# Performance work log

Hardware: AMD Instinct MI355X
Metric: run time of the kernel (lower is better)

## Reference

```python
import jax, jax.numpy as jnp
import numpy as np

N, D_MODEL, D_PE, H = 4096, 512, 16, 8


def setup_inputs() -> dict:
    key = jax.random.key(0)
    ks = jax.random.split(key, 6)
    s = 1.0 / np.sqrt(D_MODEL)
    return {
        "x": jax.random.normal(ks[0], (N, D_MODEL), dtype=jnp.float32),
        "pe": jax.random.normal(ks[1], (N, D_PE), dtype=jnp.float32),
        "w_qkv": jax.random.normal(ks[2], (D_MODEL, 3 * D_MODEL), dtype=jnp.float32) * s,
        "b_qkv": jnp.zeros((3 * D_MODEL,), dtype=jnp.float32),
        "w_pe": jax.random.normal(ks[3], (D_PE, H), dtype=jnp.float32) * (1.0 / np.sqrt(D_PE)),
        "b_pe": jnp.zeros((H,), dtype=jnp.float32),
        "w_out": jax.random.normal(ks[4], (D_MODEL, D_MODEL), dtype=jnp.float32) * s,
        "b_out": jnp.zeros((D_MODEL,), dtype=jnp.float32),
    }


def reference(x, pe, w_qkv, b_qkv, w_pe, b_pe, w_out, b_out):
    n, d = x.shape
    h = w_pe.shape[1]
    hd = d // h
    scale = hd ** -0.5

    qkv = (x @ w_qkv + b_qkv).reshape(n, 3, h, hd)  # [N,3,H,hd]
    q = jnp.transpose(qkv[:, 0], (1, 0, 2))  # [H,N,hd]
    k = jnp.transpose(qkv[:, 1], (1, 0, 2))
    v = jnp.transpose(qkv[:, 2], (1, 0, 2))

    pe_proj = pe @ w_pe + b_pe  # [N,H]
    # bias[h,i,j] = pe_proj[j,h] - pe_proj[i,h]  (matches torch unsqueeze/permute)
    pt = pe_proj.T  # [H,N]
    bias = pt[:, None, :] - pt[:, :, None]  # [H,N,N]

    scores = jnp.einsum('hnd,hmd->hnm', q, k) * scale + bias  # [H,N,N]
    attn = jax.nn.softmax(scores, axis=-1)
    out = jnp.einsum('hnm,hmd->hnd', attn, v)  # [H,N,hd]
    out = jnp.transpose(out, (1, 0, 2)).reshape(n, d)
    return out @ w_out + b_out
```

## Files before the change

### kernel.cpp

```cpp
#include <hip/hip_runtime.h>
#include <stdint.h>
#include <stddef.h>


typedef unsigned short u16;
typedef __attribute__((ext_vector_type(8))) short short8;
typedef __attribute__((ext_vector_type(8))) unsigned short us8;
typedef __attribute__((ext_vector_type(4))) unsigned short us4;
typedef __attribute__((ext_vector_type(4))) float floatx4;

__device__ __forceinline__ u16 f2b(float f) {
  union { float f; uint32_t u; } v; v.f = f;
  uint32_t u = v.u;
  return (u16)((u + 0x7fffu + ((u >> 16) & 1u)) >> 16);
}

__device__ __forceinline__ uint32_t pkbf16(float a, float b) {
  union { float f; uint32_t u; } x, y; x.f = a; y.f = b;
  return __builtin_amdgcn_perm(y.u + 0x8000u, x.u + 0x8000u, 0x07060302u);
}

#if __has_builtin(__builtin_amdgcn_exp2f)
__device__ __forceinline__ float fexp2(float x) { return __builtin_amdgcn_exp2f(x); }
#else
__device__ __forceinline__ float fexp2(float x) { return exp2f(x); }
#endif

__device__ __forceinline__ void gld16(const u16* g, u16* l) {
  __builtin_amdgcn_global_load_lds(
      (const __attribute__((address_space(1))) uint32_t*)(const void*)g,
      (__attribute__((address_space(3))) uint32_t*)(void*)l, 16, 0, 0);
}


__device__ __forceinline__ void tr_tile(const float* __restrict__ in,
                                        u16* __restrict__ out, int R, int C,
                                        int bx, int by, u16 (*tile)[33]) {
  int tx = threadIdx.x & 31, ty = threadIdx.x >> 5;
  int c0 = bx * 32, r0 = by * 32;
#pragma unroll
  for (int i = 0; i < 32; i += 8)
    tile[ty + i][tx] = f2b(in[(size_t)(r0 + ty + i) * C + c0 + tx]);
  __syncthreads();
#pragma unroll
  for (int i = 0; i < 32; i += 8)
    out[(size_t)(c0 + ty + i) * R + r0 + tx] = tile[tx][ty + i];
}

__global__ __launch_bounds__(256) void k_prep(
    const float* __restrict__ x, u16* __restrict__ xb,
    const float* __restrict__ w_qkv, u16* __restrict__ wqkvT,
    const float* __restrict__ w_out, u16* __restrict__ woutT,
    const float* __restrict__ pe, const float* __restrict__ w_pe,
    const float* __restrict__ b_pe, float* __restrict__ wexp,
    u16* __restrict__ wpb) {
  __shared__ u16 tile[32][33];
  int b = blockIdx.x;
  if (b < 2048) {
    int i = b * 256 + threadIdx.x;
    float4 v = ((const float4*)x)[i];
    uint2 o = make_uint2(pkbf16(v.x, v.y), pkbf16(v.z, v.w));
    ((uint2*)xb)[i] = o;
  } else if (b < 2816) {
    int idx = b - 2048;
    tr_tile(w_qkv, wqkvT, 512, 1536, idx % 48, idx / 48, tile);
  } else if (b < 3072) {
    int idx = b - 2816;
    tr_tile(w_out, woutT, 512, 512, idx % 16, idx / 16, tile);
  } else {
    int idx = (b - 3072) * 256 + threadIdx.x;
    int h = idx >> 12, n = idx & 4095;
    float acc = b_pe[h];
#pragma unroll
    for (int d = 0; d < 16; ++d) acc = fmaf(pe[n * 16 + d], w_pe[d * 8 + h], acc);
    float w = exp2f(acc * 1.4426950408889634f - 16.0f);
    u16 wb = f2b(w);
    union { uint32_t u; float f; } cv; cv.u = ((uint32_t)wb) << 16;
    wexp[h * 4096 + n] = cv.f;
    int pn = (n & ~31) | (((n >> 2) & 3) << 3) | (((n >> 4) & 1) << 2) | (n & 3);
    wpb[h * 4096 + pn] = wb;
  }
}


__global__ __launch_bounds__(512, 6) void k_gemm_qkv(const u16* __restrict__ A,
                                                     const u16* __restrict__ Bt,
                                                     const float* __restrict__ bias,
                                                     const float* __restrict__ wexp,
                                                     u16* __restrict__ qk,
                                                     u16* __restrict__ vtp) {
  __shared__ __align__(16) u16 smem[24576];
  const int tid = threadIdx.x;
  const int lane = tid & 63, wave = tid >> 6;
  const int colx = lane & 15, quad = lane >> 4;
  const int m0 = blockIdx.y * 64, n0 = blockIdx.x * 128;
  const int wm = wave >> 2, wn = wave & 3;
  const int sc = (lane & 7) ^ ((lane >> 3) & 7);
  const floatx4 fz = {0.f, 0.f, 0.f, 0.f};
  floatx4 acc[2][2];
#pragma unroll
  for (int i = 0; i < 2; ++i)
#pragma unroll
    for (int j = 0; j < 2; ++j) acc[i][j] = fz;

#define PREF_QKV(k0, b)                                                       \
  {                                                                           \
    int rowa = wave * 8 + (lane >> 3);                                        \
    gld16(&A[(size_t)(m0 + rowa) * 512 + (k0) + sc * 8],                      \
          &smem[(b) * 4096 + wave * 512 + lane * 8]);                         \
    _Pragma("unroll") for (int c = 0; c < 2; ++c) {                           \
      int rowb = wave * 16 + c * 8 + (lane >> 3);                             \
      gld16(&Bt[(size_t)(n0 + rowb) * 512 + (k0) + sc * 8],                   \
            &smem[8192 + (b) * 8192 + wave * 1024 + c * 512 + lane * 8]);     \
    }                                                                         \
  }

  PREF_QKV(0, 0);
  __syncthreads();
  for (int it = 0; it < 8; ++it) {
    int cur = it & 1;
    if (it < 7) PREF_QKV((it + 1) * 64, cur ^ 1);
    const u16* As = &smem[cur * 4096];
    const u16* Bs = &smem[8192 + cur * 8192];
#pragma unroll
    for (int kk = 0; kk < 2; ++kk) {
      short8 af[2], bf[2];
#pragma unroll
      for (int i = 0; i < 2; ++i) {
        int row = wm * 32 + i * 16 + colx;
        af[i] = *(const short8*)&As[row * 64 + (((kk * 4 + quad) ^ (colx & 7))) * 8];
      }
#pragma unroll
      for (int j = 0; j < 2; ++j) {
        int row = wn * 32 + j * 16 + colx;
        bf[j] = *(const short8*)&Bs[row * 64 + (((kk * 4 + quad) ^ (colx & 7))) * 8];
      }
#pragma unroll
      for (int i = 0; i < 2; ++i)
#pragma unroll
        for (int j = 0; j < 2; ++j)
          acc[i][j] = __builtin_amdgcn_mfma_f32_16x16x32_bf16(af[i], bf[j], acc[i][j], 0, 0, 0);
    }
    __syncthreads();
  }

  const bool isV = (blockIdx.x >= 8);
  if (!isV) {
#pragma unroll
    for (int j = 0; j < 2; ++j) {
      int c = n0 + wn * 32 + j * 16 + colx;
      float bq = bias[c];
      float qs = (c < 512) ? 0.18033688011112042f : 1.0f;
#pragma unroll
      for (int i = 0; i < 2; ++i)
#pragma unroll
        for (int r = 0; r < 4; ++r) {
          int row = m0 + wm * 32 + i * 16 + quad * 4 + r;
          qk[(size_t)row * 1024 + c] = f2b((acc[i][j][r] + bq) * qs);
        }
    }
  } else {
    const int dv = n0 - 1024;
    u16* Vl = smem;
    const int hh = (dv + wn * 32) >> 6;
#pragma unroll
    for (int j = 0; j < 2; ++j) {
      float bq = bias[n0 + wn * 32 + j * 16 + colx];
#pragma unroll
      for (int i = 0; i < 2; ++i) {
        floatx4 wv = *(const floatx4*)&wexp[hh * 4096 + m0 + wm * 32 + i * 16 + quad * 4];
        us4 o;
#pragma unroll
        for (int r = 0; r < 4; ++r) o[r] = f2b((acc[i][j][r] + bq) * wv[r]);
        int dl = wn * 32 + j * 16 + colx;
        int nc = wm * 32 + quad * 8 + i * 4;
        *(us4*)&Vl[dl * 72 + nc] = o;
      }
    }
    __syncthreads();
#pragma unroll
    for (int t = 0; t < 2; ++t) {
      int idx = t * 512 + tid;
      int dl = idx >> 3, ch = idx & 7;
      *(us8*)&vtp[(size_t)(dv + dl) * 4096 + m0 + ch * 8] =
          *(const us8*)&Vl[dl * 72 + ch * 8];
    }
  }
#undef PREF_QKV
}


__global__ __launch_bounds__(512, 8) void k_flash(const u16* __restrict__ qk,
                                                  const u16* __restrict__ vt,
                                                  const u16* __restrict__ wpb,
                                                  float* __restrict__ opart,
                                                  float* __restrict__ lpart) {
  __shared__ __align__(16) u16 smem[20480];
  float* bufs = (float*)smem;

  const int tid = threadIdx.x;
  const int lane = tid & 63, wave = tid >> 6;
  const int colx = lane & 15, quad = lane >> 4;
  const int ih = wave >> 1, jq = wave & 1;
  const int q0 = blockIdx.x * 64;
  const int h = blockIdx.y;
  const int z = blockIdx.z;
  const int kvb = z * 2048;
  const floatx4 fz = {0.f, 0.f, 0.f, 0.f};

  const int sc = (lane & 7) ^ ((lane >> 3) & 7);
  const int srow = wave * 8 + (lane >> 3);

  {
    int row = tid >> 3, ch = tid & 7;
    *(us8*)&smem[row * 64 + (ch ^ (row & 7)) * 8] =
        *(const us8*)&qk[(size_t)(q0 + row) * 1024 + h * 64 + ch * 8];
  }
  const u16* qptr = qk + (size_t)(kvb + srow) * 1024 + 512 + h * 64 + sc * 8;
  const u16* vptr = vt + (size_t)(h * 64 + srow) * 4096 + kvb + sc * 8;
  const u16* wptr = wpb + h * 4096 + kvb + jq * 32 + quad * 8;
  gld16(qptr, &smem[4096 + wave * 512 + lane * 8]);
  gld16(vptr, &smem[12288 + wave * 512 + lane * 8]);
  qptr += 65536;
  vptr += 64;
  __syncthreads();

  short8 qf[2];
#pragma unroll
  for (int kk = 0; kk < 2; ++kk) {
    int row = ih * 16 + colx;
    qf[kk] = *(const short8*)&smem[row * 64 + (((kk * 4 + quad) ^ (colx & 7))) * 8];
  }

  floatx4 oacc[4], lacc = fz;
#pragma unroll
  for (int cb = 0; cb < 4; ++cb) oacc[cb] = fz;

#define FBODY(CUR, PREF)                                                      \
  {                                                                           \
    short8 wf = *(const short8*)wptr;                                         \
    wptr += 64;                                                               \
    if (PREF) {                                                               \
      gld16(qptr, &smem[4096 + (1 - (CUR)) * 4096 + wave * 512 + lane * 8]);  \
      gld16(vptr, &smem[12288 + (1 - (CUR)) * 4096 + wave * 512 + lane * 8]); \
      qptr += 65536;                                                          \
      vptr += 64;                                                             \
    }                                                                         \
    const u16* Ks = &smem[4096 + (CUR) * 4096];                               \
    const u16* Vts = &smem[12288 + (CUR) * 4096];                             \
    floatx4 sacc[2] = {fz, fz};                                               \
    _Pragma("unroll") for (int j2 = 0; j2 < 2; ++j2) {                        \
      _Pragma("unroll") for (int kk = 0; kk < 2; ++kk) {                      \
        int row = jq * 32 + j2 * 16 + colx;                                   \
        short8 kf = *(const short8*)&Ks[row * 64 +                            \
                                        (((kk * 4 + quad) ^ (colx & 7))) * 8];\
        sacc[j2] =                                                            \
            __builtin_amdgcn_mfma_f32_16x16x32_bf16(kf, qf[kk], sacc[j2], 0, 0, 0); \
      }                                                                       \
    }                                                                         \
    union { uint32_t w[4]; short8 s; } pk;                                    \
    _Pragma("unroll") for (int j2 = 0; j2 < 2; ++j2) {                        \
      float p0 = fexp2(sacc[j2][0]);                                          \
      float p1 = fexp2(sacc[j2][1]);                                          \
      float p2 = fexp2(sacc[j2][2]);                                          \
      float p3 = fexp2(sacc[j2][3]);                                          \
      pk.w[j2 * 2 + 0] = pkbf16(p0, p1);                                      \
      pk.w[j2 * 2 + 1] = pkbf16(p2, p3);                                      \
    }                                                                         \
    _Pragma("unroll") for (int cb = 0; cb < 4; ++cb) {                        \
      int row = cb * 16 + colx;                                               \
      short8 vf = *(const short8*)&Vts[row * 64 +                             \
                                       (((jq * 4 + quad) ^ (colx & 7))) * 8]; \
      oacc[cb] =                                                              \
          __builtin_amdgcn_mfma_f32_16x16x32_bf16(pk.s, vf, oacc[cb], 0, 0, 0); \
    }                                                                         \
    lacc = __builtin_amdgcn_mfma_f32_16x16x32_bf16(pk.s, wf, lacc, 0, 0, 0);  \
    __syncthreads();                                                          \
  }

  for (int t = 0; t < 15; ++t) {
    FBODY(0, 1)
    FBODY(1, 1)
  }
  FBODY(0, 1)
  FBODY(1, 0)
#undef FBODY

  float* b = bufs + ih * 1040;
  if (jq == 1) {
#pragma unroll
    for (int cb = 0; cb < 4; ++cb)
#pragma unroll
      for (int r = 0; r < 4; ++r)
        b[(quad * 4 + r) * 65 + cb * 16 + colx] = oacc[cb][r];
    if (colx == 0)
#pragma unroll
      for (int r = 0; r < 4; ++r) b[(quad * 4 + r) * 65 + 64] = lacc[r];
  }
  __syncthreads();
  if (jq == 0) {
#pragma unroll
    for (int cb = 0; cb < 4; ++cb)
#pragma unroll
      for (int r = 0; r < 4; ++r)
        oacc[cb][r] += b[(quad * 4 + r) * 65 + cb * 16 + colx];
#pragma unroll
    for (int r = 0; r < 4; ++r) lacc[r] += b[(quad * 4 + r) * 65 + 64];
    float* op = opart + (size_t)z * 2097152;
#pragma unroll
    for (int cb = 0; cb < 4; ++cb)
#pragma unroll
      for (int r = 0; r < 4; ++r)
        op[(size_t)(q0 + ih * 16 + quad * 4 + r) * 512 + h * 64 + cb * 16 + colx] =
            oacc[cb][r];
    if (colx == 0)
#pragma unroll
      for (int r = 0; r < 4; ++r)
        lpart[z * 32768 + h * 4096 + q0 + ih * 16 + quad * 4 + r] = lacc[r];
  }
}


__global__ __launch_bounds__(256) void k_comb(const float* __restrict__ opart,
                                              const float* __restrict__ lpart,
                                              u16* __restrict__ ao) {
  int idx = blockIdx.x * 256 + threadIdx.x;
  int n = idx >> 7, d4 = idx & 127;
  int h = d4 >> 4;
  float l = lpart[h * 4096 + n] + lpart[32768 + h * 4096 + n];
  float inv = 1.0f / l;
  float4 o0 = *(const float4*)&opart[(size_t)n * 512 + d4 * 4];
  float4 o1 = *(const float4*)&opart[2097152 + (size_t)n * 512 + d4 * 4];
  us4 o;
  o[0] = f2b((o0.x + o1.x) * inv);
  o[1] = f2b((o0.y + o1.y) * inv);
  o[2] = f2b((o0.z + o1.z) * inv);
  o[3] = f2b((o0.w + o1.w) * inv);
  *(us4*)&ao[(size_t)n * 512 + d4 * 4] = o;
}


__global__ __launch_bounds__(512, 4) void k_gemm_out(const u16* __restrict__ A,
                                                     const u16* __restrict__ Bt,
                                                     const float* __restrict__ bias,
                                                     float* __restrict__ Cout) {
  __shared__ __align__(16) u16 smem[16384];
  const int tid = threadIdx.x;
  const int lane = tid & 63, wave = tid >> 6;
  const int colx = lane & 15, quad = lane >> 4;
  const int m0 = blockIdx.y * 64, n0 = blockIdx.x * 64;
  const int wm = wave >> 2, wn = wave & 3;
  const int sc = (lane & 7) ^ ((lane >> 3) & 7);
  const floatx4 fz = {0.f, 0.f, 0.f, 0.f};
  floatx4 acc[2];
  acc[0] = fz; acc[1] = fz;

#define PREF_OUT(k0, b)                                                       \
  {                                                                           \
    int rowa = wave * 8 + (lane >> 3);                                        \
    gld16(&A[(size_t)(m0 + rowa) * 512 + (k0) + sc * 8],                      \
          &smem[(b) * 4096 + wave * 512 + lane * 8]);                         \
    gld16(&Bt[(size_t)(n0 + rowa) * 512 + (k0) + sc * 8],                     \
          &smem[8192 + (b) * 4096 + wave * 512 + lane * 8]);                  \
  }

  PREF_OUT(0, 0);
  __syncthreads();
  for (int it = 0; it < 8; ++it) {
    int cur = it & 1;
    if (it < 7) PREF_OUT((it + 1) * 64, cur ^ 1);
    const u16* As = &smem[cur * 4096];
    const u16* Bs = &smem[8192 + cur * 4096];
#pragma unroll
    for (int kk = 0; kk < 2; ++kk) {
      short8 af[2], bf;
#pragma unroll
      for (int i = 0; i < 2; ++i) {
        int row = wm * 32 + i * 16 + colx;
        af[i] = *(const short8*)&As[row * 64 + (((kk * 4 + quad) ^ (colx & 7))) * 8];
      }
      {
        int row = wn * 16 + colx;
        bf = *(const short8*)&Bs[row * 64 + (((kk * 4 + quad) ^ (colx & 7))) * 8];
      }
#pragma unroll
      for (int i = 0; i < 2; ++i)
        acc[i] = __builtin_amdgcn_mfma_f32_16x16x32_bf16(af[i], bf, acc[i], 0, 0, 0);
    }
    __syncthreads();
  }
  int c = n0 + wn * 16 + colx;
  float bq = bias[c];
#pragma unroll
  for (int i = 0; i < 2; ++i)
#pragma unroll
    for (int r = 0; r < 4; ++r) {
      int row = m0 + wm * 32 + i * 16 + quad * 4 + r;
      Cout[(size_t)row * 512 + c] = acc[i][r] + bq;
    }
#undef PREF_OUT
}


extern "C" void kernel_launch(void* const* d_in, const int* in_sizes, int n_in,
                              void* d_out, int out_size, void* d_ws, size_t ws_size,
                              hipStream_t stream) {
  const float* x     = (const float*)d_in[0];
  const float* pe    = (const float*)d_in[1];
  const float* w_qkv = (const float*)d_in[2];
  const float* b_qkv = (const float*)d_in[3];
  const float* w_pe  = (const float*)d_in[4];
  const float* b_pe  = (const float*)d_in[5];
  const float* w_out = (const float*)d_in[6];
  const float* b_out = (const float*)d_in[7];
  float* out = (float*)d_out;

  u16* xb    = (u16*)d_ws;
  u16* wqkvT = xb    + 2097152;
  u16* woutT = wqkvT + 786432;
  u16* qk    = woutT + 262144;
  u16* vt    = qk    + 4194304;
  u16* wpb   = vt    + 2097152;
  u16* ao    = wpb   + 32768;
  float* wexp  = (float*)(ao + 2097152);
  float* opart = wexp + 32768;
  float* lpart = opart + 4194304;

  k_prep<<<3200, 256, 0, stream>>>(x, xb, w_qkv, wqkvT, w_out, woutT,
                                   pe, w_pe, b_pe, wexp, wpb);
  k_gemm_qkv<<<dim3(12, 64), 512, 0, stream>>>(xb, wqkvT, b_qkv, wexp, qk, vt);
  k_flash<<<dim3(64, 8, 2), 512, 0, stream>>>(qk, vt, wpb, opart, lpart);
  k_comb<<<2048, 256, 0, stream>>>(opart, lpart, ao);
  k_gemm_out<<<dim3(8, 64), 512, 0, stream>>>(ao, woutT, b_out, out);
}
```

Measured before the change: 143.7 us.

## Drop KV split and combine kernel, software-pipeline PV with triple buffering

The flash kernel no longer splits the KV range across two blocks. It processes all 4096 keys in one block and normalizes and writes bf16 output directly, which removes the k_comb kernel and the fp32 partial buffers. The loop is restructured with triple-buffered K/V in shared memory, the PV MFMA of the previous tile overlapped with the QK of the current tile, and s_setprio hints added. The QKV GEMM epilogue is also changed to stage Q/K through LDS for coalesced 16-byte stores. In exchange, the grid shrinks to 512 blocks, half of the previous 1024, and occupancy is lowered via launch bounds and larger LDS, which may hurt latency hiding.

```diff
diff --git a/kernel.cpp b/kernel.cpp
--- a/kernel.cpp
+++ b/kernel.cpp
@@ -146,6 +146,7 @@
 
   const bool isV = (blockIdx.x >= 8);
   if (!isV) {
+    u16* Ql = smem;
 #pragma unroll
     for (int j = 0; j < 2; ++j) {
       int c = n0 + wn * 32 + j * 16 + colx;
@@ -155,9 +156,18 @@
       for (int i = 0; i < 2; ++i)
 #pragma unroll
         for (int r = 0; r < 4; ++r) {
-          int row = m0 + wm * 32 + i * 16 + quad * 4 + r;
-          qk[(size_t)row * 1024 + c] = f2b((acc[i][j][r] + bq) * qs);
+          int rl = wm * 32 + i * 16 + quad * 4 + r;
+          int cl = wn * 32 + j * 16 + colx;
+          Ql[rl * 136 + cl] = f2b((acc[i][j][r] + bq) * qs);
         }
+    }
+    __syncthreads();
+#pragma unroll
+    for (int t = 0; t < 2; ++t) {
+      int idx = t * 512 + tid;
+      int rl = idx >> 4, ch = idx & 15;
+      *(us8*)&qk[(size_t)(m0 + rl) * 1024 + n0 + ch * 8] =
+          *(const us8*)&Ql[rl * 136 + ch * 8];
     }
   } else {
     const int dv = n0 - 1024;
@@ -190,12 +200,11 @@
 }
 
 
-__global__ __launch_bounds__(512, 8) void k_flash(const u16* __restrict__ qk,
+__global__ __launch_bounds__(512, 4) void k_flash(const u16* __restrict__ qk,
                                                   const u16* __restrict__ vt,
                                                   const u16* __restrict__ wpb,
-                                                  float* __restrict__ opart,
-                                                  float* __restrict__ lpart) {
-  __shared__ __align__(16) u16 smem[20480];
+                                                  u16* __restrict__ ao) {
+  __shared__ __align__(16) u16 smem[28672];
   float* bufs = (float*)smem;
 
   const int tid = threadIdx.x;
@@ -204,8 +213,6 @@
   const int ih = wave >> 1, jq = wave & 1;
   const int q0 = blockIdx.x * 64;
   const int h = blockIdx.y;
-  const int z = blockIdx.z;
-  const int kvb = z * 2048;
   const floatx4 fz = {0.f, 0.f, 0.f, 0.f};
 
   const int sc = (lane & 7) ^ ((lane >> 3) & 7);
@@ -216,11 +223,11 @@
     *(us8*)&smem[row * 64 + (ch ^ (row & 7)) * 8] =
         *(const us8*)&qk[(size_t)(q0 + row) * 1024 + h * 64 + ch * 8];
   }
-  const u16* qptr = qk + (size_t)(kvb + srow) * 1024 + 512 + h * 64 + sc * 8;
-  const u16* vptr = vt + (size_t)(h * 64 + srow) * 4096 + kvb + sc * 8;
-  const u16* wptr = wpb + h * 4096 + kvb + jq * 32 + quad * 8;
+  const u16* qptr = qk + (size_t)srow * 1024 + 512 + h * 64 + sc * 8;
+  const u16* vptr = vt + (size_t)(h * 64 + srow) * 4096 + sc * 8;
+  const u16* wptr = wpb + h * 4096 + jq * 32 + quad * 8;
   gld16(qptr, &smem[4096 + wave * 512 + lane * 8]);
-  gld16(vptr, &smem[12288 + wave * 512 + lane * 8]);
+  gld16(vptr, &smem[16384 + wave * 512 + lane * 8]);
   qptr += 65536;
   vptr += 64;
   __syncthreads();
@@ -236,55 +243,78 @@
 #pragma unroll
   for (int cb = 0; cb < 4; ++cb) oacc[cb] = fz;
 
-#define FBODY(CUR, PREF)                                                      \
+  union { uint32_t w[4]; short8 s; } pkp;
+  short8 wfp;
+
+#define FBODY(KR, VW, VR, PREF, DOPV)                                         \
   {                                                                           \
-    short8 wf = *(const short8*)wptr;                                         \
+    short8 wfc = *(const short8*)wptr;                              \
     wptr += 64;                                                               \
     if (PREF) {                                                               \
-      gld16(qptr, &smem[4096 + (1 - (CUR)) * 4096 + wave * 512 + lane * 8]);  \
-      gld16(vptr, &smem[12288 + (1 - (CUR)) * 4096 + wave * 512 + lane * 8]); \
+      gld16(qptr, &smem[4096 + (VW) * 4096 + wave * 512 + lane * 8]);         \
+      gld16(vptr, &smem[16384 + (VW) * 4096 + wave * 512 + lane * 8]);        \
       qptr += 65536;                                                          \
       vptr += 64;                                                             \
     }                                                                         \
-    const u16* Ks = &smem[4096 + (CUR) * 4096];                               \
-    const u16* Vts = &smem[12288 + (CUR) * 4096];                             \
+    __builtin_amdgcn_s_setprio(1);                                            \
+    if (DOPV) {          \
+      const u16* Vts = &smem[16384 + (VR) * 4096];                            \
+      _Pragma("unroll") for (int cb = 0; cb < 4; ++cb) {                      \
+        int row = cb * 16 + colx;                                             \
+        short8 vf = *(const short8*)&Vts[row * 64 +                           \
+                                         (((jq * 4 + quad) ^ (colx & 7))) * 8]; \
+        oacc[cb] = __builtin_amdgcn_mfma_f32_16x16x32_bf16(                   \
+            pkp.s, vf, oacc[cb], 0, 0, 0);                                    \
+      }                                                                       \
+      lacc = __builtin_amdgcn_mfma_f32_16x16x32_bf16(pkp.s, wfp, lacc, 0, 0, 0); \
+    }                                                                         \
+    const u16* Ks = &smem[4096 + (KR) * 4096];                                \
     floatx4 sacc[2] = {fz, fz};                                               \
     _Pragma("unroll") for (int j2 = 0; j2 < 2; ++j2) {                        \
       _Pragma("unroll") for (int kk = 0; kk < 2; ++kk) {                      \
         int row = jq * 32 + j2 * 16 + colx;                                   \
         short8 kf = *(const short8*)&Ks[row * 64 +                            \
                                         (((kk * 4 + quad) ^ (colx & 7))) * 8];\
-        sacc[j2] =                                                            \
-            __builtin_amdgcn_mfma_f32_16x16x32_bf16(kf, qf[kk], sacc[j2], 0, 0, 0); \
+        sacc[j2] = __builtin_amdgcn_mfma_f32_16x16x32_bf16(                   \
+            kf, qf[kk], sacc[j2], 0, 0, 0);                                   \
       }                                                                       \
     }                                                                         \
-    union { uint32_t w[4]; short8 s; } pk;                                    \
+    __builtin_amdgcn_s_setprio(0);                                            \
     _Pragma("unroll") for (int j2 = 0; j2 < 2; ++j2) {                        \
       float p0 = fexp2(sacc[j2][0]);                                          \
       float p1 = fexp2(sacc[j2][1]);                                          \
       float p2 = fexp2(sacc[j2][2]);                                          \
       float p3 = fexp2(sacc[j2][3]);                                          \
-      pk.w[j2 * 2 + 0] = pkbf16(p0, p1);                                      \
-      pk.w[j2 * 2 + 1] = pkbf16(p2, p3);                                      \
+      pkp.w[j2 * 2 + 0] = pkbf16(p0, p1);                                     \
+      pkp.w[j2 * 2 + 1] = pkbf16(p2, p3);                                     \
     }                                                                         \
-    _Pragma("unroll") for (int cb = 0; cb < 4; ++cb) {                        \
-      int row = cb * 16 + colx;                                               \
-      short8 vf = *(const short8*)&Vts[row * 64 +                             \
-                                       (((jq * 4 + quad) ^ (colx & 7))) * 8]; \
-      oacc[cb] =                                                              \
-          __builtin_amdgcn_mfma_f32_16x16x32_bf16(pk.s, vf, oacc[cb], 0, 0, 0); \
-    }                                                                         \
-    lacc = __builtin_amdgcn_mfma_f32_16x16x32_bf16(pk.s, wf, lacc, 0, 0, 0);  \
+    wfp = wfc;                                                                \
     __syncthreads();                                                          \
   }
 
-  for (int t = 0; t < 15; ++t) {
-    FBODY(0, 1)
-    FBODY(1, 1)
-  }
-  FBODY(0, 1)
-  FBODY(1, 0)
+  FBODY(0, 1, 0, 1, 0)
+  for (int t = 0; t < 20; ++t) {
+    FBODY(1, 2, 0, 1, 1)
+    FBODY(2, 0, 1, 1, 1)
+    FBODY(0, 1, 2, 1, 1)
+  }
+  FBODY(1, 2, 0, 1, 1)
+  FBODY(2, 0, 1, 1, 1)
+  FBODY(0, 0, 2, 0, 1)
 #undef FBODY
+
+  {
+    const u16* Vts = &smem[16384 + 0 * 4096];
+#pragma unroll
+    for (int cb = 0; cb < 4; ++cb) {
+      int row = cb * 16 + colx;
+      short8 vf = *(const short8*)&Vts[row * 64 +
+                                       (((jq * 4 + quad) ^ (colx & 7))) * 8];
+      oacc[cb] = __builtin_amdgcn_mfma_f32_16x16x32_bf16(pkp.s, vf, oacc[cb], 0, 0, 0);
+    }
+    lacc = __builtin_amdgcn_mfma_f32_16x16x32_bf16(pkp.s, wfp, lacc, 0, 0, 0);
+  }
+  __syncthreads();
 
   float* b = bufs + ih * 1040;
   if (jq == 1) {
@@ -306,37 +336,18 @@
         oacc[cb][r] += b[(quad * 4 + r) * 65 + cb * 16 + colx];
 #pragma unroll
     for (int r = 0; r < 4; ++r) lacc[r] += b[(quad * 4 + r) * 65 + 64];
-    float* op = opart + (size_t)z * 2097152;
+    float inv[4];
+#pragma unroll
+    for (int r = 0; r < 4; ++r) inv[r] = 1.0f / lacc[r];
 #pragma unroll
     for (int cb = 0; cb < 4; ++cb)
 #pragma unroll
-      for (int r = 0; r < 4; ++r)
-        op[(size_t)(q0 + ih * 16 + quad * 4 + r) * 512 + h * 64 + cb * 16 + colx] =
-            oacc[cb][r];
-    if (colx == 0)
-#pragma unroll
-      for (int r = 0; r < 4; ++r)
-        lpart[z * 32768 + h * 4096 + q0 + ih * 16 + quad * 4 + r] = lacc[r];
-  }
-}
-
-
-__global__ __launch_bounds__(256) void k_comb(const float* __restrict__ opart,
-                                              const float* __restrict__ lpart,
-                                              u16* __restrict__ ao) {
-  int idx = blockIdx.x * 256 + threadIdx.x;
-  int n = idx >> 7, d4 = idx & 127;
-  int h = d4 >> 4;
-  float l = lpart[h * 4096 + n] + lpart[32768 + h * 4096 + n];
-  float inv = 1.0f / l;
-  float4 o0 = *(const float4*)&opart[(size_t)n * 512 + d4 * 4];
-  float4 o1 = *(const float4*)&opart[2097152 + (size_t)n * 512 + d4 * 4];
-  us4 o;
-  o[0] = f2b((o0.x + o1.x) * inv);
-  o[1] = f2b((o0.y + o1.y) * inv);
-  o[2] = f2b((o0.z + o1.z) * inv);
-  o[3] = f2b((o0.w + o1.w) * inv);
-  *(us4*)&ao[(size_t)n * 512 + d4 * 4] = o;
+      for (int r = 0; r < 4; ++r) {
+        int row = q0 + ih * 16 + quad * 4 + r;
+        ao[(size_t)row * 512 + h * 64 + cb * 16 + colx] =
+            f2b(oacc[cb][r] * inv[r]);
+      }
+  }
 }
 
 
@@ -423,13 +434,10 @@
   u16* wpb   = vt    + 2097152;
   u16* ao    = wpb   + 32768;
   float* wexp  = (float*)(ao + 2097152);
-  float* opart = wexp + 32768;
-  float* lpart = opart + 4194304;
 
   k_prep<<<3200, 256, 0, stream>>>(x, xb, w_qkv, wqkvT, w_out, woutT,
                                    pe, w_pe, b_pe, wexp, wpb);
   k_gemm_qkv<<<dim3(12, 64), 512, 0, stream>>>(xb, wqkvT, b_qkv, wexp, qk, vt);
-  k_flash<<<dim3(64, 8, 2), 512, 0, stream>>>(qk, vt, wpb, opart, lpart);
-  k_comb<<<2048, 256, 0, stream>>>(opart, lpart, ao);
+  k_flash<<<dim3(64, 8), 512, 0, stream>>>(qk, vt, wpb, ao);
   k_gemm_out<<<dim3(8, 64), 512, 0, stream>>>(ao, woutT, b_out, out);
 }
```

Measured after the change: 143.2 us. No clear change (-0.4%).
